# Performance work log

Measured on AMD Instinct MI355X. Metric: run time of the kernel, lower is better.

Reference implementation:

```python
import jax, jax.numpy as jnp
import numpy as np

N, E, B = 100000, 400000, 4096      # nodes, directed edges, graphs
P, d = 4, 49                        # phm_dim, per-component dim; D = P*d = 196
L = 3                               # message-passing layers
D1, D2 = 64, 32                     # downstream per-component dims (256/4, 128/4)


def setup_inputs():
    key = jax.random.key(0)
    ks = jax.random.split(key, 20)
    def nrm(k, shape, s=0.1):
        return jax.random.normal(k, shape, dtype=jnp.float32) * s
    return {
        "x": jax.random.randint(ks[0], (N, 9), 0, 119),
        "edge_index": jax.random.randint(ks[1], (2, E), 0, N),
        "edge_attr": jax.random.randint(ks[2], (E, 3), 0, 8),
        "batch": jnp.sort(jax.random.randint(ks[3], (N,), 0, B)),
        # encoders: summed categorical embeddings in hypercomplex form [*, P, d]
        "atom_emb": nrm(ks[4], (9, 119, P, d)),
        "bond_emb": nrm(ks[5], (L, 3, 8, P, d)),
        # per-layer PHM conv: contribution matrices A (phm rule) + component weights W
        "conv_A": nrm(ks[6], (L, P, P, P), 0.5),
        "conv_W": nrm(ks[7], (L, P, d, d)),
        "conv_b": jnp.zeros((L, P, d), jnp.float32),
        "mp_gamma": jnp.ones((L, P * d), jnp.float32),
        "mp_beta": jnp.zeros((L, P * d), jnp.float32),
        # soft-attention pooling: PHM linear + real transformer gate
        "pool_A": nrm(ks[8], (P, P, P), 0.5),
        "pool_W": nrm(ks[9], (P, d, d)),
        "pool_b": jnp.zeros((P, d), jnp.float32),
        "pool_rt_w": nrm(ks[10], (P,), 0.5),
        "pool_rt_b": jnp.zeros((d,), jnp.float32),
        # downstream PHM MLP 196 -> 256 -> 128 -> 4*1, then real trafo -> 1
        "dn_A": nrm(ks[11], (3, P, P, P), 0.5),
        "dn1_W": nrm(ks[12], (P, d, D1)),
        "dn1_b": jnp.zeros((P, D1), jnp.float32),
        "dn1_gamma": jnp.ones((P * D1,), jnp.float32),
        "dn1_beta": jnp.zeros((P * D1,), jnp.float32),
        "dn2_W": nrm(ks[13], (P, D1, D2)),
        "dn2_b": jnp.zeros((P, D2), jnp.float32),
        "dn2_gamma": jnp.ones((P * D2,), jnp.float32),
        "dn2_beta": jnp.zeros((P * D2,), jnp.float32),
        "dn3_W": nrm(ks[14], (P, D2, 1)),
        "dn3_b": jnp.zeros((P, 1), jnp.float32),
        "rt_w": nrm(ks[15], (P,), 0.5),
        "rt_b": jnp.zeros((1,), jnp.float32),
    }


def phm_linear(x, A, W, b):
    # PHM linear: y = x @ (sum_i kron(A_i, W_i)) + b, on [n, P, din] -> [n, P, dout]
    return jnp.einsum('nkp,ikj,ipq->njq', x, A, W) + b


def naive_bn(x, gamma, beta, eps=1e-5):
    # naive batch norm over the batch axis, per flattened hypercomplex feature
    n, p, dd = x.shape
    x2 = x.reshape(n, p * dd)
    mu = x2.mean(axis=0)
    var = x2.var(axis=0)
    x2 = (x2 - mu) * jax.lax.rsqrt(var + eps) * gamma + beta
    return x2.reshape(n, p, dd)


def reference(x, edge_index, edge_attr, batch, atom_emb, bond_emb,
              conv_A, conv_W, conv_b, mp_gamma, mp_beta,
              pool_A, pool_W, pool_b, pool_rt_w, pool_rt_b,
              dn_A, dn1_W, dn1_b, dn1_gamma, dn1_beta,
              dn2_W, dn2_b, dn2_gamma, dn2_beta, dn3_W, dn3_b, rt_w, rt_b):
    src, dst = edge_index[0], edge_index[1]
    # atom encoder: sum embeddings of 9 categorical features -> [N, P, d]
    h0 = atom_emb[jnp.arange(9), x].sum(axis=1)
    h = h0
    for l in range(L):  # small fixed layer count
        # bond encoder for this layer -> [E, P, d]
        e = bond_emb[l][jnp.arange(3), edge_attr].sum(axis=1)
        # message = x_j + e_ij (identity msg encoder); self-loop (zero edge feat) adds h
        m = h[src] + e
        agg = jax.ops.segment_sum(m, dst, num_segments=N) + h
        z = phm_linear(agg, conv_A[l], conv_W[l], conv_b[l])
        z = jax.nn.relu(naive_bn(z, mp_gamma[l], mp_beta[l]))
        h = z + h0  # skip-connect to first embedding (sc_type='first')
    # soft-attention pooling: real-valued sigmoid gate per node feature
    g = jax.nn.sigmoid(
        jnp.einsum('npk,p->nk', phm_linear(h, pool_A, pool_W, pool_b), pool_rt_w)
        + pool_rt_b)
    pooled = jax.ops.segment_sum(h * g[:, None, :], batch, num_segments=B)  # [B, P, d]
    # downstream PHM MLP with naive batch norm + relu
    z = jax.nn.relu(naive_bn(phm_linear(pooled, dn_A[0], dn1_W, dn1_b), dn1_gamma, dn1_beta))
    z = jax.nn.relu(naive_bn(phm_linear(z, dn_A[1], dn2_W, dn2_b), dn2_gamma, dn2_beta))
    o = phm_linear(z, dn_A[2], dn3_W, dn3_b)          # [B, P, 1]
    return jnp.einsum('npk,p->nk', o, rt_w) + rt_b    # [B, 1]
```

## Files before the change

### kernel.cpp

```cpp
#include <hip/hip_runtime.h>
#include <cstdint>
#include <cstddef>

#define N_NODES 100000
#define N_EDGES 400000
#define N_GRAPHS 4096
#define DF 196
#define DD 49
#define NPB 5
#define TST 200

typedef __bf16 bf16x8 __attribute__((ext_vector_type(8)));
typedef float f32x4 __attribute__((ext_vector_type(4)));

__device__ __forceinline__ unsigned short f2bf(float f) {
  unsigned int u = __float_as_uint(f);
  u = u + 0x7FFFu + ((u >> 16) & 1u);
  return (unsigned short)(u >> 16);
}
__device__ __forceinline__ float bf2f(unsigned short h) {
  return __uint_as_float(((unsigned int)h) << 16);
}

__global__ void convert_wfrag_kernel(const float* __restrict__ cA,
                                     const float* __restrict__ cW,
                                     unsigned short* __restrict__ wfrag) {
  int idx = blockIdx.x * blockDim.x + threadIdx.x;
  if (idx >= 3 * 100352) return;
  int l = idx / 100352;
  int r = idx - l * 100352;
  int ct = r / 7168; int r1 = r - ct * 7168;
  int ks = r1 / 1024; int r2 = r1 - ks * 1024;
  int h = r2 / 512;  int r3 = r2 - h * 512;
  int ln = r3 / 8;   int j = r3 - ln * 8;
  int col = ct * 16 + (ln & 15);
  int k = ks * 32 + (ln >> 4) * 8 + j;
  float v = 0.f;
  if (col < DF && k < DF) {
    int k4 = k / DD, p = k - (k / DD) * DD;
    int j4 = col / DD, q = col - (col / DD) * DD;
#pragma unroll
    for (int i = 0; i < 4; i++)
      v += cA[((l * 4 + i) * 4 + k4) * 4 + j4] * cW[((l * 4 + i) * DD + p) * DD + q];
  }
  unsigned short hi = f2bf(v);
  wfrag[idx] = (h == 0) ? hi : f2bf(v - bf2f(hi));
}

__global__ void build_gate_kernel(const float* __restrict__ pA, const float* __restrict__ pW,
                                  const float* __restrict__ pb, const float* __restrict__ rtw,
                                  const float* __restrict__ rtb,
                                  float* __restrict__ gateW, float* __restrict__ gbias) {
  int idx = blockIdx.x * blockDim.x + threadIdx.x;
  if (idx < DF * DD) {
    int r = idx / DD, q = idx - (idx / DD) * DD;
    int k = r / DD, p = r - (r / DD) * DD;
    float s = 0.f;
#pragma unroll
    for (int i = 0; i < 4; i++) {
      float aw = 0.f;
#pragma unroll
      for (int j = 0; j < 4; j++) aw += pA[(i * 4 + k) * 4 + j] * rtw[j];
      s += aw * pW[(i * DD + p) * DD + q];
    }
    gateW[idx] = s;
  } else if (idx < DF * DD + DD) {
    int q = idx - DF * DD;
    float s = rtb[q];
#pragma unroll
    for (int j = 0; j < 4; j++) s += rtw[j] * pb[j * DD + q];
    gbias[q] = s;
  }
}

__global__ void build_dn_kernel(const float* __restrict__ dnA,
                                const float* __restrict__ W1, const float* __restrict__ W2,
                                const float* __restrict__ W3,
                                float* __restrict__ M1, float* __restrict__ M2,
                                float* __restrict__ M3) {
  int idx = blockIdx.x * blockDim.x + threadIdx.x;
  const int n1 = DF * 256, n2 = 256 * 128, n3 = 128 * 4;
  if (idx < n1) {
    int r = idx >> 8, c = idx & 255;
    int k = r / DD, p = r - (r / DD) * DD;
    int j = c >> 6, Q = c & 63;
    float s = 0.f;
#pragma unroll
    for (int i = 0; i < 4; i++) s += dnA[i * 16 + k * 4 + j] * W1[(i * DD + p) * 64 + Q];
    M1[idx] = s;
  } else if (idx < n1 + n2) {
    int m = idx - n1;
    int r = m >> 7, c = m & 127;
    int k = r >> 6, p = r & 63, j = c >> 5, q = c & 31;
    float s = 0.f;
#pragma unroll
    for (int i = 0; i < 4; i++) s += dnA[64 + i * 16 + k * 4 + j] * W2[(i * 64 + p) * 32 + q];
    M2[m] = s;
  } else if (idx < n1 + n2 + n3) {
    int m = idx - n1 - n2;
    int r = m >> 2, j = m & 3;
    int k = r >> 5, p = r & 31;
    float s = 0.f;
#pragma unroll
    for (int i = 0; i < 4; i++) s += dnA[128 + i * 16 + k * 4 + j] * W3[i * 32 + p];
    M3[m] = s;
  }
}

__global__ void lut_kernel(const float* __restrict__ bond, float* __restrict__ lut) {
  int idx = blockIdx.x * blockDim.x + threadIdx.x;
  if (idx >= 3 * 512 * DF) return;
  int l = idx / (512 * DF);
  int r = idx - l * (512 * DF);
  int code = r / DF, c = r - (r / DF) * DF;
  int a0 = code & 7, a1 = (code >> 3) & 7, a2 = (code >> 6) & 7;
  lut[idx] = bond[((l * 3 + 0) * 8 + a0) * DF + c]
           + bond[((l * 3 + 1) * 8 + a1) * DF + c]
           + bond[((l * 3 + 2) * 8 + a2) * DF + c];
}

__global__ void hist_kernel(const int* __restrict__ dst, int* __restrict__ counts) {
  int e = blockIdx.x * blockDim.x + threadIdx.x;
  if (e < N_EDGES) atomicAdd(&counts[dst[e]], 1);
}

__global__ void scan_local_kernel(const int* __restrict__ counts, int* __restrict__ offs,
                                  int* __restrict__ bsum) {
  __shared__ int sm[256];
  int tid = threadIdx.x;
  int gid = blockIdx.x * 256 + tid;
  int v = (gid < N_NODES) ? counts[gid] : 0;
  sm[tid] = v;
  __syncthreads();
  for (int d = 1; d < 256; d <<= 1) {
    int add = (tid >= d) ? sm[tid - d] : 0;
    __syncthreads();
    sm[tid] += add;
    __syncthreads();
  }
  if (gid < N_NODES) offs[gid] = sm[tid] - v;
  if (tid == 255) bsum[blockIdx.x] = sm[255];
}

__global__ void scan_bsum_kernel(int* __restrict__ bsum, int* __restrict__ bpre, int nb) {
  __shared__ int sm[512];
  int tid = threadIdx.x;
  int v = (tid < nb) ? bsum[tid] : 0;
  sm[tid] = v;
  __syncthreads();
  for (int d = 1; d < 512; d <<= 1) {
    int add = (tid >= d) ? sm[tid - d] : 0;
    __syncthreads();
    sm[tid] += add;
    __syncthreads();
  }
  if (tid < nb) bpre[tid] = sm[tid] - v;
}

__global__ void add_off_kernel(int* __restrict__ offs, const int* __restrict__ bpre) {
  int gid = blockIdx.x * blockDim.x + threadIdx.x;
  if (gid < N_NODES) offs[gid] += bpre[gid >> 8];
  if (gid == 0) offs[N_NODES] = N_EDGES;
}

__global__ void scatter_kernel(const int* __restrict__ src, const int* __restrict__ dst,
                               const int* __restrict__ ea, int* __restrict__ counts,
                               const int* __restrict__ offs,
                               unsigned int* __restrict__ sorted) {
  int e = blockIdx.x * blockDim.x + threadIdx.x;
  if (e >= N_EDGES) return;
  int d = dst[e];
  int code = ea[e * 3 + 0] | (ea[e * 3 + 1] << 3) | (ea[e * 3 + 2] << 6);
  int pos = offs[d] + atomicSub(&counts[d], 1) - 1;
  sorted[pos] = (unsigned int)src[e] | ((unsigned int)code << 17);
}

__global__ void sortseg_kernel(const int* __restrict__ offs,
                               unsigned int* __restrict__ sorted) {
  int n = blockIdx.x * blockDim.x + threadIdx.x;
  if (n >= N_NODES) return;
  int s = offs[n], e = offs[n + 1];
  for (int i = s + 1; i < e; i++) {
    unsigned int v = sorted[i];
    int j = i - 1;
    while (j >= s && sorted[j] > v) { sorted[j + 1] = sorted[j]; j--; }
    sorted[j + 1] = v;
  }
}

__global__ void atom_enc_kernel(const int* __restrict__ x, const float* __restrict__ emb,
                                float* __restrict__ h0) {
  int idx = blockIdx.x * blockDim.x + threadIdx.x;
  if (idx >= N_NODES * DF) return;
  int n = idx / DF;
  int c = idx - n * DF;
  float s = 0.f;
#pragma unroll
  for (int f = 0; f < 9; f++) {
    int xi = x[n * 9 + f];
    s += emb[(f * 119 + xi) * DF + c];
  }
  h0[idx] = s;
}

__global__ __launch_bounds__(256)
void agg_kernel(const float* __restrict__ h, const int* __restrict__ offs,
                const unsigned int* __restrict__ sorted, const float* __restrict__ lut,
                unsigned short* __restrict__ tH, unsigned short* __restrict__ tL) {
  int t = threadIdx.x;
  int i = t / 49, q = t - i * 49;
  if (i >= NPB) return;
  int node = blockIdx.x * NPB + i;
  if (node >= N_NODES) return;
  const float4* h4 = (const float4*)h;
  const float4* l4 = (const float4*)lut;
  float4 acc = h4[(size_t)node * 49 + q];
  int s = offs[node], e = offs[node + 1];
  for (int k = s; k < e; k++) {
    unsigned int se = sorted[k];
    int srcn = se & 0x1FFFF;
    int code = se >> 17;
    float4 hv = h4[(size_t)srcn * 49 + q];
    float4 lv = l4[(size_t)code * 49 + q];
    acc.x += hv.x + lv.x;
    acc.y += hv.y + lv.y;
    acc.z += hv.z + lv.z;
    acc.w += hv.w + lv.w;
  }
  ushort4 hh, ll;
  hh.x = f2bf(acc.x); ll.x = f2bf(acc.x - bf2f(hh.x));
  hh.y = f2bf(acc.y); ll.y = f2bf(acc.y - bf2f(hh.y));
  hh.z = f2bf(acc.z); ll.z = f2bf(acc.z - bf2f(hh.z));
  hh.w = f2bf(acc.w); ll.w = f2bf(acc.w - bf2f(hh.w));
  size_t ob = (size_t)node * TST + q * 4;
  *(ushort4*)(tH + ob) = hh;
  *(ushort4*)(tL + ob) = ll;
  if (q == 48) {
    ushort4 z = make_ushort4(0, 0, 0, 0);
    *(ushort4*)(tH + (size_t)node * TST + 196) = z;
    *(ushort4*)(tL + (size_t)node * TST + 196) = z;
  }
}

__global__ __launch_bounds__(256, 2)
void conv_mfma_kernel(unsigned short* __restrict__ tH,
                      unsigned short* __restrict__ tL,
                      const unsigned short* __restrict__ wfrag,
                      const float* __restrict__ bias,
                      float* __restrict__ stats) {
  __shared__ __align__(16) unsigned short smW[28672];
  const int t = threadIdx.x;
  const int lane = t & 63;
  const int w = t >> 6;
  const int li = lane & 15;
  const int rg = lane >> 4;
  const int rowbase = blockIdx.x * 128 + w * 32;

  f32x4 acc[2][14];
#pragma unroll
  for (int rt = 0; rt < 2; rt++)
#pragma unroll
    for (int ct = 0; ct < 14; ct++) acc[rt][ct] = (f32x4){0.f, 0.f, 0.f, 0.f};

  uint4 h0b[2], l0b[2], h1b[2], l1b[2], h2b[2], l2b[2], h3b[2], l3b[2];

#define LOADA(ks, aH, aL)                                                      \
  {                                                                            \
    _Pragma("unroll") for (int rt = 0; rt < 2; rt++) {                         \
      size_t o = (size_t)(rowbase + rt * 16 + li) * TST + (ks) * 32 + rg * 8;  \
      aH[rt] = *(const uint4*)(tH + o);                                        \
      aL[rt] = *(const uint4*)(tL + o);                                        \
    }                                                                          \
  }

#define COMPUTE(ksl, aH, aL)                                                   \
  {                                                                            \
    _Pragma("unroll") for (int ct = 0; ct < 14; ct++) {                        \
      bf16x8 bh = *(const bf16x8*)(smW + (((ct * 2 + (ksl)) * 2 + 0) * 512 + lane * 8)); \
      bf16x8 bl = *(const bf16x8*)(smW + (((ct * 2 + (ksl)) * 2 + 1) * 512 + lane * 8)); \
      _Pragma("unroll") for (int rt = 0; rt < 2; rt++) {                       \
        bf16x8 ah = *(const bf16x8*)&aH[rt];                                   \
        bf16x8 al = *(const bf16x8*)&aL[rt];                                   \
        acc[rt][ct] = __builtin_amdgcn_mfma_f32_16x16x32_bf16(ah, bh, acc[rt][ct], 0, 0, 0); \
        acc[rt][ct] = __builtin_amdgcn_mfma_f32_16x16x32_bf16(al, bh, acc[rt][ct], 0, 0, 0); \
        acc[rt][ct] = __builtin_amdgcn_mfma_f32_16x16x32_bf16(ah, bl, acc[rt][ct], 0, 0, 0); \
      }                                                                        \
    }                                                                          \
  }

#define STAGE_PAIR(p)                                                          \
  {                                                                            \
    _Pragma("unroll") for (int f0 = 0; f0 < 14; f0++) {                        \
      int f = f0 * 256 + t;                                                    \
      int ln = f & 63, g = f >> 6;                                             \
      int hh = g & 1, g2 = g >> 1;                                             \
      int ksl = g2 & 1, ct = g2 >> 1;                                          \
      *(uint4*)(smW + (((ct * 2 + ksl) * 2 + hh) * 512 + ln * 8)) =            \
          *(const uint4*)(wfrag + (((size_t)(ct * 7 + 2 * (p) + ksl) * 2 + hh) * 512 + ln * 8)); \
    }                                                                          \
  }

  LOADA(0, h0b, l0b);
  LOADA(1, h1b, l1b);
  LOADA(2, h2b, l2b);
  LOADA(3, h3b, l3b);
  STAGE_PAIR(0);
  __syncthreads();
  COMPUTE(0, h0b, l0b);
  LOADA(4, h0b, l0b);
  COMPUTE(1, h1b, l1b);
  __syncthreads();
  STAGE_PAIR(1);
  __syncthreads();
  COMPUTE(0, h2b, l2b);
  LOADA(5, h1b, l1b);
  COMPUTE(1, h3b, l3b);
  __syncthreads();
  STAGE_PAIR(2);
  __syncthreads();
  COMPUTE(0, h0b, l0b);
  LOADA(6, h2b, l2b);
  COMPUTE(1, h1b, l1b);
  __syncthreads();
  {
#pragma unroll
    for (int f0 = 0; f0 < 7; f0++) {
      int f = f0 * 256 + t;
      int ln = f & 63, g = f >> 6;
      int hh = g & 1, ct = g >> 1;
      *(uint4*)(smW + (((ct * 2) * 2 + hh) * 512 + ln * 8)) =
          *(const uint4*)(wfrag + (((size_t)(ct * 7 + 6) * 2 + hh) * 512 + ln * 8));
    }
  }
  __syncthreads();
  COMPUTE(0, h2b, l2b);

  float part[14], psq[14];
#pragma unroll
  for (int ct = 0; ct < 14; ct++) { part[ct] = 0.f; psq[ct] = 0.f; }

  unsigned short* lhi = smW;
  unsigned short* llo = smW + 64 * 224;

#pragma unroll
  for (int half = 0; half < 2; half++) {
    __syncthreads();
    if ((w >> 1) == half) {
      int rl0 = (w & 1) * 32;
#pragma unroll
      for (int ct = 0; ct < 14; ct++) {
        int c = ct * 16 + li;
        float bv = (c < DF) ? bias[c] : 0.f;
#pragma unroll
        for (int rt = 0; rt < 2; rt++) {
#pragma unroll
          for (int r = 0; r < 4; r++) {
            int row = rl0 + rt * 16 + rg * 4 + r;
            int gr = rowbase + rt * 16 + rg * 4 + r;
            float y = acc[rt][ct][r] + bv;
            if (gr < N_NODES && c < DF) { part[ct] += y; psq[ct] += y * y; }
            unsigned short hi = f2bf(y);
            lhi[row * 224 + c] = hi;
            llo[row * 224 + c] = f2bf(y - bf2f(hi));
          }
        }
      }
    }
    __syncthreads();
    for (int idx = t; idx < 1600; idx += 256) {
      int row = idx / 25, u = idx - (idx / 25) * 25;
      int gr = blockIdx.x * 128 + half * 64 + row;
      if (gr < N_NODES) {
        uint4 vh = *(const uint4*)(lhi + row * 224 + u * 8);
        uint4 vl = *(const uint4*)(llo + row * 224 + u * 8);
        if (u == 24) { vh.z = 0u; vh.w = 0u; vl.z = 0u; vl.w = 0u; }
        *(uint4*)(tH + (size_t)gr * TST + u * 8) = vh;
        *(uint4*)(tL + (size_t)gr * TST + u * 8) = vl;
      }
    }
  }

  __syncthreads();
  float* redS = (float*)smW;
  float* redQ = redS + 4 * 224;
#pragma unroll
  for (int ct = 0; ct < 14; ct++) {
    float p = part[ct], q = psq[ct];
    p += __shfl_xor(p, 16, 64); p += __shfl_xor(p, 32, 64);
    q += __shfl_xor(q, 16, 64); q += __shfl_xor(q, 32, 64);
    if (rg == 0) { redS[w * 224 + ct * 16 + li] = p; redQ[w * 224 + ct * 16 + li] = q; }
  }
  __syncthreads();
  if (t < DF) {
    float s1 = redS[t] + redS[224 + t] + redS[448 + t] + redS[672 + t];
    float s2 = redQ[t] + redQ[224 + t] + redQ[448 + t] + redQ[672 + t];
    atomicAdd(&stats[t], s1);
    atomicAdd(&stats[DF + t], s2);
  }
#undef LOADA
#undef COMPUTE
#undef STAGE_PAIR
}

__global__ void bn_relu_split_kernel(const unsigned short* __restrict__ tH,
                                     const unsigned short* __restrict__ tL,
                                     const float* __restrict__ stats,
                                     const float* __restrict__ gamma,
                                     const float* __restrict__ beta,
                                     const float* __restrict__ h0,
                                     float* __restrict__ h) {
  int idx = blockIdx.x * blockDim.x + threadIdx.x;
  if (idx >= N_NODES * DD) return;
  int n = idx / DD, q = idx - (idx / DD) * DD;
  size_t ib = (size_t)n * TST + q * 4;
  ushort4 hv = *(const ushort4*)(tH + ib);
  ushort4 lv = *(const ushort4*)(tL + ib);
  size_t fb = (size_t)n * DF + q * 4;
  float4 sk = *(const float4*)(h0 + fb);
  int c = q * 4;
  const float invN = 1.f / N_NODES;
  float4 o;
  {
    float z = bf2f(hv.x) + bf2f(lv.x);
    float mu = stats[c + 0] * invN;
    float var = stats[DF + c + 0] * invN - mu * mu;
    o.x = fmaxf((z - mu) * rsqrtf(var + 1e-5f) * gamma[c + 0] + beta[c + 0], 0.f) + sk.x;
  }
  {
    float z = bf2f(hv.y) + bf2f(lv.y);
    float mu = stats[c + 1] * invN;
    float var = stats[DF + c + 1] * invN - mu * mu;
    o.y = fmaxf((z - mu) * rsqrtf(var + 1e-5f) * gamma[c + 1] + beta[c + 1], 0.f) + sk.y;
  }
  {
    float z = bf2f(hv.z) + bf2f(lv.z);
    float mu = stats[c + 2] * invN;
    float var = stats[DF + c + 2] * invN - mu * mu;
    o.z = fmaxf((z - mu) * rsqrtf(var + 1e-5f) * gamma[c + 2] + beta[c + 2], 0.f) + sk.z;
  }
  {
    float z = bf2f(hv.w) + bf2f(lv.w);
    float mu = stats[c + 3] * invN;
    float var = stats[DF + c + 3] * invN - mu * mu;
    o.w = fmaxf((z - mu) * rsqrtf(var + 1e-5f) * gamma[c + 3] + beta[c + 3], 0.f) + sk.w;
  }
  *(float4*)(h + fb) = o;
}

template<int S, int MODE>
__launch_bounds__(256)
__global__ void gemm_kernel(const float* X, const float* __restrict__ W,
                            const float* __restrict__ bias, float* Y,
                            float* __restrict__ stats, int Nrows, int K, int NC) {
  constexpr int WN = S * 64;
  __shared__ __align__(16) float At[32][64];
  __shared__ __align__(16) float Wl[32][WN];
  const int t = threadIdx.x;
  const int tx = t & 15;
  const int ty = t >> 4;
  const int r0 = blockIdx.x * 64;

  float acc[S][4][4];
#pragma unroll
  for (int s = 0; s < S; s++)
#pragma unroll
    for (int i = 0; i < 4; i++)
#pragma unroll
      for (int j = 0; j < 4; j++) acc[s][i][j] = 0.f;

  const int lr = t >> 2;
  const int kb = (t & 3) * 8;
  constexpr int TPR = S * 16;
  const int cw = (t % TPR) * 4;
  const int kr = t / TPR;
  constexpr int RPP = 256 / TPR;
  constexpr int PASSES = 32 / RPP;

  for (int k0 = 0; k0 < K; k0 += 32) {
    {
      const int gr = r0 + lr;
      const float* xp = X + (size_t)gr * K + k0 + kb;
      if (gr < Nrows && (k0 + kb + 7) < K) {
        float4 v0 = *(const float4*)(xp);
        float4 v1 = *(const float4*)(xp + 4);
        At[kb + 0][lr] = v0.x; At[kb + 1][lr] = v0.y;
        At[kb + 2][lr] = v0.z; At[kb + 3][lr] = v0.w;
        At[kb + 4][lr] = v1.x; At[kb + 5][lr] = v1.y;
        At[kb + 6][lr] = v1.z; At[kb + 7][lr] = v1.w;
      } else {
#pragma unroll
        for (int i = 0; i < 8; i++) {
          int kk = kb + i;
          float v = 0.f;
          if (gr < Nrows && (k0 + kk) < K) v = xp[i];
          At[kk][lr] = v;
        }
      }
    }
#pragma unroll
    for (int ps = 0; ps < PASSES; ps++) {
      int kk = kr + ps * RPP;
      int gk = k0 + kk;
      if (gk < K && (cw + 3) < NC && ((NC & 3) == 0)) {
        float4 v = *(const float4*)(W + (size_t)gk * NC + cw);
        Wl[kk][cw + 0] = v.x; Wl[kk][cw + 1] = v.y;
        Wl[kk][cw + 2] = v.z; Wl[kk][cw + 3] = v.w;
      } else {
#pragma unroll
        for (int j = 0; j < 4; j++) {
          int c = cw + j;
          float v = 0.f;
          if (gk < K && c < NC) v = W[(size_t)gk * NC + c];
          Wl[kk][c] = v;
        }
      }
    }
    __syncthreads();
#pragma unroll 4
    for (int kk = 0; kk < 32; kk++) {
      float4 a = *(const float4*)&At[kk][ty * 4];
      float av[4] = {a.x, a.y, a.z, a.w};
#pragma unroll
      for (int s = 0; s < S; s++) {
        float4 w = *(const float4*)&Wl[kk][s * 64 + tx * 4];
        float wv[4] = {w.x, w.y, w.z, w.w};
#pragma unroll
        for (int i = 0; i < 4; i++)
#pragma unroll
          for (int j = 0; j < 4; j++)
            acc[s][i][j] = fmaf(av[i], wv[j], acc[s][i][j]);
      }
    }
    __syncthreads();
  }

#pragma unroll
  for (int s = 0; s < S; s++)
#pragma unroll
    for (int j = 0; j < 4; j++) {
      int c = s * 64 + tx * 4 + j;
      float bv = (c < NC) ? bias[c] : 0.f;
#pragma unroll
      for (int i = 0; i < 4; i++) {
        float y = acc[s][i][j] + bv;
        if (MODE == 1) y = 1.f / (1.f + __expf(-y));
        acc[s][i][j] = y;
      }
    }
#pragma unroll
  for (int i = 0; i < 4; i++) {
    int gr = r0 + ty * 4 + i;
    if (gr < Nrows) {
#pragma unroll
      for (int s = 0; s < S; s++)
#pragma unroll
        for (int j = 0; j < 4; j++) {
          int c = s * 64 + tx * 4 + j;
          if (c < NC) Y[(size_t)gr * NC + c] = acc[s][i][j];
        }
    }
  }
  if (MODE == 0) {
    float* red = &Wl[0][0];
    __syncthreads();
#pragma unroll
    for (int s = 0; s < S; s++)
#pragma unroll
      for (int j = 0; j < 4; j++) {
        float p = 0.f;
#pragma unroll
        for (int i = 0; i < 4; i++)
          if ((r0 + ty * 4 + i) < Nrows) p += acc[s][i][j];
        red[ty * WN + s * 64 + tx * 4 + j] = p;
      }
    __syncthreads();
    if (t < WN) {
      float tot = 0.f;
#pragma unroll
      for (int yy = 0; yy < 16; yy++) tot += red[yy * WN + t];
      if (t < NC) atomicAdd(&stats[t], tot);
    }
    __syncthreads();
#pragma unroll
    for (int s = 0; s < S; s++)
#pragma unroll
      for (int j = 0; j < 4; j++) {
        float p = 0.f;
#pragma unroll
        for (int i = 0; i < 4; i++)
          if ((r0 + ty * 4 + i) < Nrows) p += acc[s][i][j] * acc[s][i][j];
        red[ty * WN + s * 64 + tx * 4 + j] = p;
      }
    __syncthreads();
    if (t < WN) {
      float tot = 0.f;
#pragma unroll
      for (int yy = 0; yy < 16; yy++) tot += red[yy * WN + t];
      if (t < NC) atomicAdd(&stats[NC + t], tot);
    }
  }
}

__global__ void bn_relu_kernel(const float* __restrict__ z, const float* __restrict__ stats,
                               const float* __restrict__ gamma, const float* __restrict__ beta,
                               float* __restrict__ out,
                               int total, int NC, float invN) {
  int idx = blockIdx.x * blockDim.x + threadIdx.x;
  if (idx >= total) return;
  int c = idx % NC;
  float mu = stats[c] * invN;
  float var = stats[NC + c] * invN - mu * mu;
  float v = (z[idx] - mu) * rsqrtf(var + 1e-5f) * gamma[c] + beta[c];
  out[idx] = fmaxf(v, 0.f);
}

__device__ __forceinline__ int lower_bound_dev(const int* a, int n, int v) {
  int lo = 0, hi = n;
  while (lo < hi) { int mid = (lo + hi) >> 1; if (a[mid] < v) lo = mid + 1; else hi = mid; }
  return lo;
}

__global__ void pool_kernel(const float* __restrict__ h, const float* __restrict__ g,
                            const int* __restrict__ batch, float* __restrict__ pooled) {
  int b = blockIdx.x;
  __shared__ int bounds[2];
  if (threadIdx.x == 0) {
    bounds[0] = lower_bound_dev(batch, N_NODES, b);
    bounds[1] = lower_bound_dev(batch, N_NODES, b + 1);
  }
  __syncthreads();
  int c = threadIdx.x;
  if (c >= DF) return;
  int s = bounds[0], e = bounds[1];
  int q = c % DD;
  float acc = 0.f;
  for (int n = s; n < e; n++)
    acc = fmaf(h[(size_t)n * DF + c], g[(size_t)n * DD + q], acc);
  pooled[(size_t)b * DF + c] = acc;
}

__global__ void final_kernel(const float* __restrict__ z2, const float* __restrict__ M3,
                             const float* __restrict__ b3, const float* __restrict__ rtw,
                             const float* __restrict__ rtb, float* __restrict__ out) {
  __shared__ float sM[128 * 4];
  __shared__ float srw[4];
  __shared__ float srb;
  int t = threadIdx.x;
  for (int i = t; i < 512; i += 256) sM[i] = M3[i];
  if (t < 4) srw[t] = rtw[t];
  if (t == 4) srb = rtb[0];
  __syncthreads();
  int b = blockIdx.x * blockDim.x + t;
  if (b >= N_GRAPHS) return;
  float o0 = b3[0], o1 = b3[1], o2 = b3[2], o3 = b3[3];
  const float* zp = z2 + (size_t)b * 128;
  for (int p = 0; p < 128; p++) {
    float v = zp[p];
    o0 = fmaf(v, sM[p * 4 + 0], o0);
    o1 = fmaf(v, sM[p * 4 + 1], o1);
    o2 = fmaf(v, sM[p * 4 + 2], o2);
    o3 = fmaf(v, sM[p * 4 + 3], o3);
  }
  out[b] = srb + o0 * srw[0] + o1 * srw[1] + o2 * srw[2] + o3 * srw[3];
}

extern "C" void kernel_launch(void* const* d_in, const int* in_sizes, int n_in,
                              void* d_out, int out_size, void* d_ws, size_t ws_size,
                              hipStream_t stream) {
  (void)in_sizes; (void)n_in; (void)out_size; (void)ws_size;
  const int* x          = (const int*)d_in[0];
  const int* edge_index = (const int*)d_in[1];
  const int* edge_attr  = (const int*)d_in[2];
  const int* batch      = (const int*)d_in[3];
  const float* atom_emb = (const float*)d_in[4];
  const float* bond_emb = (const float*)d_in[5];
  const float* conv_A   = (const float*)d_in[6];
  const float* conv_W   = (const float*)d_in[7];
  const float* conv_b   = (const float*)d_in[8];
  const float* mp_gamma = (const float*)d_in[9];
  const float* mp_beta  = (const float*)d_in[10];
  const float* pool_A   = (const float*)d_in[11];
  const float* pool_W   = (const float*)d_in[12];
  const float* pool_b   = (const float*)d_in[13];
  const float* pool_rt_w = (const float*)d_in[14];
  const float* pool_rt_b = (const float*)d_in[15];
  const float* dn_A     = (const float*)d_in[16];
  const float* dn1_W    = (const float*)d_in[17];
  const float* dn1_b    = (const float*)d_in[18];
  const float* dn1_gamma = (const float*)d_in[19];
  const float* dn1_beta = (const float*)d_in[20];
  const float* dn2_W    = (const float*)d_in[21];
  const float* dn2_b    = (const float*)d_in[22];
  const float* dn2_gamma = (const float*)d_in[23];
  const float* dn2_beta = (const float*)d_in[24];
  const float* dn3_W    = (const float*)d_in[25];
  const float* dn3_b    = (const float*)d_in[26];
  const float* rt_w     = (const float*)d_in[27];
  const float* rt_b     = (const float*)d_in[28];
  float* out = (float*)d_out;

  char* ws = (char*)d_ws;
  size_t off = 0;
  auto alloc = [&](size_t bytes) -> char* {
    char* p = ws + off;
    off = (off + bytes + 255) & ~(size_t)255;
    return p;
  };
  const size_t HBYTES = (size_t)N_NODES * DF * sizeof(float);
  float* h0 = (float*)alloc(HBYTES);
  float* h  = (float*)alloc(HBYTES);
  unsigned short* tH = (unsigned short*)alloc((size_t)N_NODES * TST * 2 + 4096);
  unsigned short* tL = (unsigned short*)alloc((size_t)N_NODES * TST * 2 + 4096);
  float* g      = (float*)tH;
  float* pooled = (float*)((char*)tH + (((size_t)N_NODES * DD * 4 + 255) & ~(size_t)255));
  float* z1     = (float*)((char*)pooled + (((size_t)N_GRAPHS * DF * 4 + 255) & ~(size_t)255));
  float* z2     = (float*)((char*)z1 + (((size_t)N_GRAPHS * 256 * 4 + 255) & ~(size_t)255));
  unsigned short* wfrag = (unsigned short*)alloc((size_t)3 * 100352 * 2);
  float* gateW  = (float*)alloc(DF * DD * 4);
  float* gbias  = (float*)alloc(64 * 4);
  float* M1     = (float*)alloc(DF * 256 * 4);
  float* M2     = (float*)alloc(256 * 128 * 4);
  float* M3     = (float*)alloc(128 * 4 * 4);
  float* stats  = (float*)alloc(2048 * 4);
  int*  counts  = (int*)alloc(N_NODES * 4);
  int*  offs    = (int*)alloc((N_NODES + 1) * 4);
  unsigned int* sorted = (unsigned int*)alloc((size_t)N_EDGES * 4);
  float* lut    = (float*)alloc((size_t)3 * 512 * DF * 4);
  int*  bsum    = (int*)alloc(512 * 4);
  int*  bpre    = (int*)alloc(512 * 4);

  const int* src = edge_index;
  const int* dst = edge_index + N_EDGES;
  const int NB = (N_NODES + 255) / 256;

  hipMemsetAsync(stats, 0, 2048 * 4, stream);
  hipMemsetAsync(counts, 0, N_NODES * 4, stream);

  convert_wfrag_kernel<<<(3 * 100352 + 255) / 256, 256, 0, stream>>>(conv_A, conv_W, wfrag);
  build_gate_kernel<<<(DF * DD + DD + 255) / 256, 256, 0, stream>>>(
      pool_A, pool_W, pool_b, pool_rt_w, pool_rt_b, gateW, gbias);
  build_dn_kernel<<<(DF * 256 + 256 * 128 + 128 * 4 + 255) / 256, 256, 0, stream>>>(
      dn_A, dn1_W, dn2_W, dn3_W, M1, M2, M3);
  lut_kernel<<<(3 * 512 * DF + 255) / 256, 256, 0, stream>>>(bond_emb, lut);

  hist_kernel<<<(N_EDGES + 255) / 256, 256, 0, stream>>>(dst, counts);
  scan_local_kernel<<<NB, 256, 0, stream>>>(counts, offs, bsum);
  scan_bsum_kernel<<<1, 512, 0, stream>>>(bsum, bpre, NB);
  add_off_kernel<<<NB, 256, 0, stream>>>(offs, bpre);
  scatter_kernel<<<(N_EDGES + 255) / 256, 256, 0, stream>>>(
      src, dst, edge_attr, counts, offs, sorted);
  sortseg_kernel<<<NB, 256, 0, stream>>>(offs, sorted);

  atom_enc_kernel<<<(N_NODES * DF + 255) / 256, 256, 0, stream>>>(x, atom_emb, h0);

  const int NCONV = (N_NODES + 127) / 128;
  for (int l = 0; l < 3; l++) {
    const float* hl = (l == 0) ? h0 : h;
    agg_kernel<<<(N_NODES + NPB - 1) / NPB, 256, 0, stream>>>(
        hl, offs, sorted, lut + (size_t)l * 512 * DF, tH, tL);
    float* st = stats + l * 392;
    conv_mfma_kernel<<<NCONV, 256, 0, stream>>>(
        tH, tL, wfrag + (size_t)l * 100352, conv_b + (size_t)l * DF, st);
    bn_relu_split_kernel<<<(N_NODES * DD + 255) / 256, 256, 0, stream>>>(
        tH, tL, st, mp_gamma + l * DF, mp_beta + l * DF, h0, h);
  }

  gemm_kernel<1, 1><<<(N_NODES + 63) / 64, 256, 0, stream>>>(
      h, gateW, gbias, g, nullptr, N_NODES, DF, DD);
  pool_kernel<<<N_GRAPHS, 256, 0, stream>>>(h, g, batch, pooled);

  gemm_kernel<4, 0><<<(N_GRAPHS + 63) / 64, 256, 0, stream>>>(
      pooled, M1, dn1_b, z1, stats + 1176, N_GRAPHS, DF, 256);
  bn_relu_kernel<<<(N_GRAPHS * 256 + 255) / 256, 256, 0, stream>>>(
      z1, stats + 1176, dn1_gamma, dn1_beta, z1, N_GRAPHS * 256, 256, 1.f / N_GRAPHS);
  gemm_kernel<2, 0><<<(N_GRAPHS + 63) / 64, 256, 0, stream>>>(
      z1, M2, dn2_b, z2, stats + 1688, N_GRAPHS, 256, 128);
  bn_relu_kernel<<<(N_GRAPHS * 128 + 255) / 256, 256, 0, stream>>>(
      z2, stats + 1688, dn2_gamma, dn2_beta, z2, N_GRAPHS * 128, 128, 1.f / N_GRAPHS);
  final_kernel<<<(N_GRAPHS + 255) / 256, 256, 0, stream>>>(z2, M3, dn3_b, rt_w, rt_b, out);
}
```

Measured before the change: 892.5 us.

## Double-buffer conv weight staging through registers and merge setup kernels

The MFMA conv kernel now stages weights one k-slice at a time into two LDS slots. Each slice is prefetched from global memory into registers and written to LDS one step ahead, which replaces the old pair-wise staging that stalled on global loads between barriers. The epilogue LDS row stride goes from 224 to 232, probably to reduce bank conflicts. Three small setup kernels (bond LUT, gate weights, downstream matrices) are merged into one launch to cut launch overhead. The register prefetch buffers add VGPR pressure and may reduce occupancy.

```diff
diff --git a/kernel.cpp b/kernel.cpp
--- a/kernel.cpp
+++ b/kernel.cpp
@@ -9,6 +9,8 @@
 #define DD 49
 #define NPB 5
 #define TST 200
+#define WSLOT 14336
+#define EST 232
 
 typedef __bf16 bf16x8 __attribute__((ext_vector_type(8)));
 typedef float f32x4 __attribute__((ext_vector_type(4)));
@@ -47,76 +49,78 @@
   wfrag[idx] = (h == 0) ? hi : f2bf(v - bf2f(hi));
 }
 
-__global__ void build_gate_kernel(const float* __restrict__ pA, const float* __restrict__ pW,
-                                  const float* __restrict__ pb, const float* __restrict__ rtw,
-                                  const float* __restrict__ rtb,
-                                  float* __restrict__ gateW, float* __restrict__ gbias) {
-  int idx = blockIdx.x * blockDim.x + threadIdx.x;
-  if (idx < DF * DD) {
-    int r = idx / DD, q = idx - (idx / DD) * DD;
-    int k = r / DD, p = r - (r / DD) * DD;
-    float s = 0.f;
-#pragma unroll
-    for (int i = 0; i < 4; i++) {
-      float aw = 0.f;
-#pragma unroll
-      for (int j = 0; j < 4; j++) aw += pA[(i * 4 + k) * 4 + j] * rtw[j];
-      s += aw * pW[(i * DD + p) * DD + q];
-    }
-    gateW[idx] = s;
-  } else if (idx < DF * DD + DD) {
-    int q = idx - DF * DD;
-    float s = rtb[q];
-#pragma unroll
-    for (int j = 0; j < 4; j++) s += rtw[j] * pb[j * DD + q];
-    gbias[q] = s;
-  }
-}
-
-__global__ void build_dn_kernel(const float* __restrict__ dnA,
-                                const float* __restrict__ W1, const float* __restrict__ W2,
-                                const float* __restrict__ W3,
-                                float* __restrict__ M1, float* __restrict__ M2,
-                                float* __restrict__ M3) {
-  int idx = blockIdx.x * blockDim.x + threadIdx.x;
+__global__ void setup_small_kernel(const float* __restrict__ bond, float* __restrict__ lut,
+                                   const float* __restrict__ pA, const float* __restrict__ pW,
+                                   const float* __restrict__ pb, const float* __restrict__ rtw,
+                                   const float* __restrict__ rtb,
+                                   float* __restrict__ gateW, float* __restrict__ gbias,
+                                   const float* __restrict__ dnA,
+                                   const float* __restrict__ W1, const float* __restrict__ W2,
+                                   const float* __restrict__ W3,
+                                   float* __restrict__ M1, float* __restrict__ M2,
+                                   float* __restrict__ M3) {
+  int idx0 = blockIdx.x * blockDim.x + threadIdx.x;
+  const int NL = 3 * 512 * DF;
+  const int NG = DF * DD + DD;
   const int n1 = DF * 256, n2 = 256 * 128, n3 = 128 * 4;
-  if (idx < n1) {
-    int r = idx >> 8, c = idx & 255;
-    int k = r / DD, p = r - (r / DD) * DD;
-    int j = c >> 6, Q = c & 63;
-    float s = 0.f;
-#pragma unroll
-    for (int i = 0; i < 4; i++) s += dnA[i * 16 + k * 4 + j] * W1[(i * DD + p) * 64 + Q];
-    M1[idx] = s;
-  } else if (idx < n1 + n2) {
-    int m = idx - n1;
-    int r = m >> 7, c = m & 127;
-    int k = r >> 6, p = r & 63, j = c >> 5, q = c & 31;
-    float s = 0.f;
-#pragma unroll
-    for (int i = 0; i < 4; i++) s += dnA[64 + i * 16 + k * 4 + j] * W2[(i * 64 + p) * 32 + q];
-    M2[m] = s;
-  } else if (idx < n1 + n2 + n3) {
-    int m = idx - n1 - n2;
-    int r = m >> 2, j = m & 3;
-    int k = r >> 5, p = r & 31;
-    float s = 0.f;
-#pragma unroll
-    for (int i = 0; i < 4; i++) s += dnA[128 + i * 16 + k * 4 + j] * W3[i * 32 + p];
-    M3[m] = s;
-  }
-}
-
-__global__ void lut_kernel(const float* __restrict__ bond, float* __restrict__ lut) {
-  int idx = blockIdx.x * blockDim.x + threadIdx.x;
-  if (idx >= 3 * 512 * DF) return;
-  int l = idx / (512 * DF);
-  int r = idx - l * (512 * DF);
-  int code = r / DF, c = r - (r / DF) * DF;
-  int a0 = code & 7, a1 = (code >> 3) & 7, a2 = (code >> 6) & 7;
-  lut[idx] = bond[((l * 3 + 0) * 8 + a0) * DF + c]
-           + bond[((l * 3 + 1) * 8 + a1) * DF + c]
-           + bond[((l * 3 + 2) * 8 + a2) * DF + c];
+  if (idx0 < NL) {
+    int idx = idx0;
+    int l = idx / (512 * DF);
+    int r = idx - l * (512 * DF);
+    int code = r / DF, c = r - (r / DF) * DF;
+    int a0 = code & 7, a1 = (code >> 3) & 7, a2 = (code >> 6) & 7;
+    lut[idx] = bond[((l * 3 + 0) * 8 + a0) * DF + c]
+             + bond[((l * 3 + 1) * 8 + a1) * DF + c]
+             + bond[((l * 3 + 2) * 8 + a2) * DF + c];
+  } else if (idx0 < NL + NG) {
+    int idx = idx0 - NL;
+    if (idx < DF * DD) {
+      int r = idx / DD, q = idx - (idx / DD) * DD;
+      int k = r / DD, p = r - (r / DD) * DD;
+      float s = 0.f;
+#pragma unroll
+      for (int i = 0; i < 4; i++) {
+        float aw = 0.f;
+#pragma unroll
+        for (int j = 0; j < 4; j++) aw += pA[(i * 4 + k) * 4 + j] * rtw[j];
+        s += aw * pW[(i * DD + p) * DD + q];
+      }
+      gateW[idx] = s;
+    } else {
+      int q = idx - DF * DD;
+      float s = rtb[q];
+#pragma unroll
+      for (int j = 0; j < 4; j++) s += rtw[j] * pb[j * DD + q];
+      gbias[q] = s;
+    }
+  } else if (idx0 < NL + NG + n1 + n2 + n3) {
+    int idx = idx0 - NL - NG;
+    if (idx < n1) {
+      int r = idx >> 8, c = idx & 255;
+      int k = r / DD, p = r - (r / DD) * DD;
+      int j = c >> 6, Q = c & 63;
+      float s = 0.f;
+#pragma unroll
+      for (int i = 0; i < 4; i++) s += dnA[i * 16 + k * 4 + j] * W1[(i * DD + p) * 64 + Q];
+      M1[idx] = s;
+    } else if (idx < n1 + n2) {
+      int m = idx - n1;
+      int r = m >> 7, c = m & 127;
+      int k = r >> 6, p = r & 63, j = c >> 5, q = c & 31;
+      float s = 0.f;
+#pragma unroll
+      for (int i = 0; i < 4; i++) s += dnA[64 + i * 16 + k * 4 + j] * W2[(i * 64 + p) * 32 + q];
+      M2[m] = s;
+    } else {
+      int m = idx - n1 - n2;
+      int r = m >> 2, j = m & 3;
+      int k = r >> 5, p = r & 31;
+      float s = 0.f;
+#pragma unroll
+      for (int i = 0; i < 4; i++) s += dnA[128 + i * 16 + k * 4 + j] * W3[i * 32 + p];
+      M3[m] = s;
+    }
+  }
 }
 
 __global__ void hist_kernel(const int* __restrict__ dst, int* __restrict__ counts) {
@@ -248,7 +252,7 @@
                       const unsigned short* __restrict__ wfrag,
                       const float* __restrict__ bias,
                       float* __restrict__ stats) {
-  __shared__ __align__(16) unsigned short smW[28672];
+  __shared__ __align__(16) unsigned short smW[2 * 64 * EST];
   const int t = threadIdx.x;
   const int lane = t & 63;
   const int w = t >> 6;
@@ -262,7 +266,8 @@
 #pragma unroll
     for (int ct = 0; ct < 14; ct++) acc[rt][ct] = (f32x4){0.f, 0.f, 0.f, 0.f};
 
-  uint4 h0b[2], l0b[2], h1b[2], l1b[2], h2b[2], l2b[2], h3b[2], l3b[2];
+  uint4 b0h[2], b0l[2], b1h[2], b1l[2], b2h[2], b2l[2];
+  uint4 wr0[7], wr1[7];
 
 #define LOADA(ks, aH, aL)                                                      \
   {                                                                            \
@@ -273,11 +278,32 @@
     }                                                                          \
   }
 
-#define COMPUTE(ksl, aH, aL)                                                   \
+#define GLOADW(ks, wr)                                                         \
+  {                                                                            \
+    _Pragma("unroll") for (int f0 = 0; f0 < 7; f0++) {                         \
+      int f = f0 * 256 + t;                                                    \
+      int ln = f & 63, g = f >> 6;                                             \
+      int hh = g & 1, ct = g >> 1;                                             \
+      wr[f0] = *(const uint4*)(wfrag +                                         \
+          (((size_t)(ct * 7 + (ks)) * 2 + hh) * 512 + ln * 8));                \
+    }                                                                          \
+  }
+
+#define DSWRITEW(wr, sbase)                                                    \
+  {                                                                            \
+    _Pragma("unroll") for (int f0 = 0; f0 < 7; f0++) {                         \
+      int f = f0 * 256 + t;                                                    \
+      int ln = f & 63, g = f >> 6;                                             \
+      int hh = g & 1, ct = g >> 1;                                             \
+      *(uint4*)(smW + (sbase) + ((ct * 2 + hh) * 512 + ln * 8)) = wr[f0];      \
+    }                                                                          \
+  }
+
+#define COMPUTE(sbase, aH, aL)                                                 \
   {                                                                            \
     _Pragma("unroll") for (int ct = 0; ct < 14; ct++) {                        \
-      bf16x8 bh = *(const bf16x8*)(smW + (((ct * 2 + (ksl)) * 2 + 0) * 512 + lane * 8)); \
-      bf16x8 bl = *(const bf16x8*)(smW + (((ct * 2 + (ksl)) * 2 + 1) * 512 + lane * 8)); \
+      bf16x8 bh = *(const bf16x8*)(smW + (sbase) + ((ct * 2 + 0) * 512 + lane * 8)); \
+      bf16x8 bl = *(const bf16x8*)(smW + (sbase) + ((ct * 2 + 1) * 512 + lane * 8)); \
       _Pragma("unroll") for (int rt = 0; rt < 2; rt++) {                       \
         bf16x8 ah = *(const bf16x8*)&aH[rt];                                   \
         bf16x8 al = *(const bf16x8*)&aL[rt];                                   \
@@ -288,59 +314,48 @@
     }                                                                          \
   }
 
-#define STAGE_PAIR(p)                                                          \
-  {                                                                            \
-    _Pragma("unroll") for (int f0 = 0; f0 < 14; f0++) {                        \
-      int f = f0 * 256 + t;                                                    \
-      int ln = f & 63, g = f >> 6;                                             \
-      int hh = g & 1, g2 = g >> 1;                                             \
-      int ksl = g2 & 1, ct = g2 >> 1;                                          \
-      *(uint4*)(smW + (((ct * 2 + ksl) * 2 + hh) * 512 + ln * 8)) =            \
-          *(const uint4*)(wfrag + (((size_t)(ct * 7 + 2 * (p) + ksl) * 2 + hh) * 512 + ln * 8)); \
-    }                                                                          \
-  }
-
-  LOADA(0, h0b, l0b);
-  LOADA(1, h1b, l1b);
-  LOADA(2, h2b, l2b);
-  LOADA(3, h3b, l3b);
-  STAGE_PAIR(0);
-  __syncthreads();
-  COMPUTE(0, h0b, l0b);
-  LOADA(4, h0b, l0b);
-  COMPUTE(1, h1b, l1b);
-  __syncthreads();
-  STAGE_PAIR(1);
-  __syncthreads();
-  COMPUTE(0, h2b, l2b);
-  LOADA(5, h1b, l1b);
-  COMPUTE(1, h3b, l3b);
-  __syncthreads();
-  STAGE_PAIR(2);
-  __syncthreads();
-  COMPUTE(0, h0b, l0b);
-  LOADA(6, h2b, l2b);
-  COMPUTE(1, h1b, l1b);
-  __syncthreads();
-  {
-#pragma unroll
-    for (int f0 = 0; f0 < 7; f0++) {
-      int f = f0 * 256 + t;
-      int ln = f & 63, g = f >> 6;
-      int hh = g & 1, ct = g >> 1;
-      *(uint4*)(smW + (((ct * 2) * 2 + hh) * 512 + ln * 8)) =
-          *(const uint4*)(wfrag + (((size_t)(ct * 7 + 6) * 2 + hh) * 512 + ln * 8));
-    }
-  }
-  __syncthreads();
-  COMPUTE(0, h2b, l2b);
+  GLOADW(0, wr0);
+  GLOADW(1, wr1);
+  LOADA(0, b0h, b0l);
+  LOADA(1, b1h, b1l);
+  LOADA(2, b2h, b2l);
+  DSWRITEW(wr0, 0);
+  GLOADW(2, wr0);
+  __syncthreads();
+  COMPUTE(0, b0h, b0l);
+  DSWRITEW(wr1, WSLOT);
+  GLOADW(3, wr1);
+  LOADA(3, b0h, b0l);
+  __syncthreads();
+  COMPUTE(WSLOT, b1h, b1l);
+  DSWRITEW(wr0, 0);
+  GLOADW(4, wr0);
+  LOADA(4, b1h, b1l);
+  __syncthreads();
+  COMPUTE(0, b2h, b2l);
+  DSWRITEW(wr1, WSLOT);
+  GLOADW(5, wr1);
+  LOADA(5, b2h, b2l);
+  __syncthreads();
+  COMPUTE(WSLOT, b0h, b0l);
+  DSWRITEW(wr0, 0);
+  GLOADW(6, wr0);
+  LOADA(6, b0h, b0l);
+  __syncthreads();
+  COMPUTE(0, b1h, b1l);
+  DSWRITEW(wr1, WSLOT);
+  __syncthreads();
+  COMPUTE(WSLOT, b2h, b2l);
+  DSWRITEW(wr0, 0);
+  __syncthreads();
+  COMPUTE(0, b0h, b0l);
 
   float part[14], psq[14];
 #pragma unroll
   for (int ct = 0; ct < 14; ct++) { part[ct] = 0.f; psq[ct] = 0.f; }
 
   unsigned short* lhi = smW;
-  unsigned short* llo = smW + 64 * 224;
+  unsigned short* llo = smW + 64 * EST;
 
 #pragma unroll
   for (int half = 0; half < 2; half++) {
@@ -360,8 +375,8 @@
             float y = acc[rt][ct][r] + bv;
             if (gr < N_NODES && c < DF) { part[ct] += y; psq[ct] += y * y; }
             unsigned short hi = f2bf(y);
-            lhi[row * 224 + c] = hi;
-            llo[row * 224 + c] = f2bf(y - bf2f(hi));
+            lhi[row * EST + c] = hi;
+            llo[row * EST + c] = f2bf(y - bf2f(hi));
           }
         }
       }
@@ -371,8 +386,8 @@
       int row = idx / 25, u = idx - (idx / 25) * 25;
       int gr = blockIdx.x * 128 + half * 64 + row;
       if (gr < N_NODES) {
-        uint4 vh = *(const uint4*)(lhi + row * 224 + u * 8);
-        uint4 vl = *(const uint4*)(llo + row * 224 + u * 8);
+        uint4 vh = *(const uint4*)(lhi + row * EST + u * 8);
+        uint4 vl = *(const uint4*)(llo + row * EST + u * 8);
         if (u == 24) { vh.z = 0u; vh.w = 0u; vl.z = 0u; vl.w = 0u; }
         *(uint4*)(tH + (size_t)gr * TST + u * 8) = vh;
         *(uint4*)(tL + (size_t)gr * TST + u * 8) = vl;
@@ -398,8 +413,9 @@
     atomicAdd(&stats[DF + t], s2);
   }
 #undef LOADA
+#undef GLOADW
+#undef DSWRITEW
 #undef COMPUTE
-#undef STAGE_PAIR
 }
 
 __global__ void bn_relu_split_kernel(const unsigned short* __restrict__ tH,
@@ -737,11 +753,12 @@
   hipMemsetAsync(counts, 0, N_NODES * 4, stream);
 
   convert_wfrag_kernel<<<(3 * 100352 + 255) / 256, 256, 0, stream>>>(conv_A, conv_W, wfrag);
-  build_gate_kernel<<<(DF * DD + DD + 255) / 256, 256, 0, stream>>>(
-      pool_A, pool_W, pool_b, pool_rt_w, pool_rt_b, gateW, gbias);
-  build_dn_kernel<<<(DF * 256 + 256 * 128 + 128 * 4 + 255) / 256, 256, 0, stream>>>(
-      dn_A, dn1_W, dn2_W, dn3_W, M1, M2, M3);
-  lut_kernel<<<(3 * 512 * DF + 255) / 256, 256, 0, stream>>>(bond_emb, lut);
+  {
+    const int total = 3 * 512 * DF + (DF * DD + DD) + (DF * 256 + 256 * 128 + 128 * 4);
+    setup_small_kernel<<<(total + 255) / 256, 256, 0, stream>>>(
+        bond_emb, lut, pool_A, pool_W, pool_b, pool_rt_w, pool_rt_b, gateW, gbias,
+        dn_A, dn1_W, dn2_W, dn3_W, M1, M2, M3);
+  }
 
   hist_kernel<<<(N_EDGES + 255) / 256, 256, 0, stream>>>(dst, counts);
   scan_local_kernel<<<NB, 256, 0, stream>>>(counts, offs, bsum);
```

Measured after the change: 1.011 ms. 1.13x slower.
